# Kernel tuning notes

Measured on AMD Instinct MI355X. Metric: run time of the kernel, lower is better.

## Reference

```python
import jax, jax.numpy as jnp
import numpy as np

B, S_ENC, S_DEC, ENC_H, DEC_H = 8, 2048, 2048, 512, 512


def setup_inputs() -> dict:
    key = jax.random.key(0)
    k1, k2, k3 = jax.random.split(key, 3)
    return {
        "enc_hidden_states": jax.random.normal(k1, (B, S_ENC, ENC_H), dtype=jnp.float32),
        "dec_hidden_states": jax.random.normal(k2, (B, S_DEC, DEC_H), dtype=jnp.float32),
        "W_att": jax.random.normal(k3, (ENC_H, DEC_H), dtype=jnp.float32),
    }


def reference(enc_hidden_states, dec_hidden_states, W_att):
    # Project encoder states: [B, S_enc, dec_h]
    enc_proj = jnp.einsum("bse,ed->bsd", enc_hidden_states, W_att)
    # Luong 'general' scores for all decoder timesteps at once: [B, S_dec, S_enc]
    # (original code loops over decoder timesteps via tf.map_fn; this is the
    # equivalent single batched matmul)
    att_logits = jnp.einsum("btd,bsd->bts", dec_hidden_states, enc_proj)
    att_softmax = jax.nn.softmax(att_logits, axis=-1)
    # Attention context vectors: [B, S_dec, enc_h]
    att_vector = jnp.einsum("bts,bse->bte", att_softmax, enc_hidden_states)
    return att_vector
```

## Files before the change

kernel.cpp:

```cpp
#include <hip/hip_runtime.h>
#include <cstdint>


#define DEVINL __device__ __forceinline__

typedef __attribute__((ext_vector_type(8))) short short8;
typedef __attribute__((ext_vector_type(4))) float f32x4;

DEVINL short f2bf(float x) {
    union { float f; uint32_t u; } v; v.f = x;
    uint32_t r = v.u + 0x7FFFu + ((v.u >> 16) & 1u);
    return (short)(r >> 16);
}
DEVINL float bf2f(short h) {
    union { uint32_t u; float f; } v; v.u = ((uint32_t)(uint16_t)h) << 16;
    return v.f;
}

DEVINL void gload_lds16(const void* g, void* l) {
    __builtin_amdgcn_global_load_lds(
        (const __attribute__((address_space(1))) char*)g,
        (__attribute__((address_space(3))) char*)l, 16, 0, 0);
}

__global__ __launch_bounds__(256)
void split_kernel(const float* __restrict__ x, short* __restrict__ hi,
                  short* __restrict__ lo)
{
    long i = ((long)blockIdx.x * 256 + threadIdx.x) * 8;
    f32x4 a = *(const f32x4*)(x + i);
    f32x4 b = *(const f32x4*)(x + i + 4);
    short8 h, l;
#pragma unroll
    for (int j = 0; j < 4; j++) {
        short ha = f2bf(a[j]); h[j] = ha;     l[j] = f2bf(a[j] - bf2f(ha));
        short hb = f2bf(b[j]); h[4 + j] = hb; l[4 + j] = f2bf(b[j] - bf2f(hb));
    }
    *(short8*)(hi + i) = h;
    *(short8*)(lo + i) = l;
}

__global__ __launch_bounds__(256)
void split_w_kernel(const float* __restrict__ w, short* __restrict__ wth,
                    short* __restrict__ wtl)
{
    int idx = blockIdx.x * 256 + threadIdx.x;
    int k = idx >> 9, n = idx & 511;
    float v = w[idx];
    short h = f2bf(v);
    wth[(long)n * 512 + k] = h;
    wtl[(long)n * 512 + k] = f2bf(v - bf2f(h));
}

__global__ __launch_bounds__(256)
void split_transpose_kernel(const float* __restrict__ x, short* __restrict__ hi,
                            short* __restrict__ lo, short* __restrict__ xt)
{
    __shared__ short tile[32][33];
    const int b  = blockIdx.z;
    const int s0 = blockIdx.x * 32;
    const int e0 = blockIdx.y * 32;
    const float* px = x + (long)b * 2048 * 512;
    short* ph = hi + (long)b * 2048 * 512;
    short* pl = lo + (long)b * 2048 * 512;
    short* pt = xt + (long)b * 512 * 2048;
    const int tx = threadIdx.x & 31;
    const int ty = threadIdx.x >> 5;
#pragma unroll
    for (int r = 0; r < 32; r += 8) {
        long idx = (long)(s0 + ty + r) * 512 + e0 + tx;
        float v = px[idx];
        short h = f2bf(v);
        ph[idx] = h;
        pl[idx] = f2bf(v - bf2f(h));
        tile[ty + r][tx] = h;
    }
    __syncthreads();
#pragma unroll
    for (int r = 0; r < 32; r += 8)
        pt[(long)(e0 + ty + r) * 2048 + s0 + tx] = tile[tx][ty + r];
}

template<int NTERMS, bool SPLIT_OUT>
__global__ __launch_bounds__(256, 2)
void gemm_bt(const short* __restrict__ Ah, const short* __restrict__ Al,
             const short* __restrict__ Bh, const short* __restrict__ Bl,
             float* __restrict__ C, short* __restrict__ Ch, short* __restrict__ Cl,
             int K, int lda, int ldb, int ldc,
             long sA, long sB, long sC)
{
    extern __shared__ char smem_raw[];
    constexpr int OPS = (NTERMS == 3) ? 4 : 2;
    constexpr int SET = 128 * 32 * OPS;
    short* smem = (short*)smem_raw;

    const int tid  = threadIdx.x;
    const int wave = tid >> 6;
    const int lane = tid & 63;
    const int quad = lane >> 4;
    const int l16  = lane & 15;
    const int wm   = (wave >> 1) * 64;
    const int wn   = (wave & 1) * 64;

    const long tile_m = (long)blockIdx.y * 128;
    const long tile_n = (long)blockIdx.x * 128;
    const int  bz     = blockIdx.z;

    const short* pAh = Ah + (long)bz * sA;
    const short* pBh = Bh + (long)bz * sB;
    const short* pAl = (NTERMS == 3) ? (Al + (long)bz * sA) : nullptr;
    const short* pBl = (NTERMS == 3) ? (Bl + (long)bz * sB) : nullptr;

    const int srow = tid >> 2;
    const int skq  = (tid & 3) * 8;
    const int lds_off = srow * 32 + skq;
    const long ga0 = (tile_m + srow) * (long)lda + skq;
    const long gb0 = (tile_n + srow) * (long)ldb + skq;

    auto stage = [&](int k0, int buf) {
        short* s   = smem + buf * SET;
        short* ash = s;
        short* bsh = s + 128 * 32;
        gload_lds16(pAh + ga0 + k0,             ash + lds_off);
        gload_lds16(pAh + ga0 + 64l * lda + k0, ash + lds_off + 64 * 32);
        gload_lds16(pBh + gb0 + k0,             bsh + lds_off);
        gload_lds16(pBh + gb0 + 64l * ldb + k0, bsh + lds_off + 64 * 32);
        if constexpr (NTERMS == 3) {
            short* asl = s + 2 * 128 * 32;
            short* bsl = s + 3 * 128 * 32;
            gload_lds16(pAl + ga0 + k0,             asl + lds_off);
            gload_lds16(pAl + ga0 + 64l * lda + k0, asl + lds_off + 64 * 32);
            gload_lds16(pBl + gb0 + k0,             bsl + lds_off);
            gload_lds16(pBl + gb0 + 64l * ldb + k0, bsl + lds_off + 64 * 32);
        }
    };

    f32x4 acc[4][4] = {};
    stage(0, 0);
    int cur = 0;

    for (int k0 = 0; k0 < K; k0 += 32) {
        __syncthreads();
        if (k0 + 32 < K) stage(k0 + 32, cur ^ 1);

        short* s   = smem + cur * SET;
        short* ash = s;
        short* bsh = s + 128 * 32;
        short* asl = s + 2 * 128 * 32;
        short* bsl = s + 3 * 128 * 32;

        short8 ah[4], bh[4], al[4], bl[4];
#pragma unroll
        for (int i = 0; i < 4; i++) {
            ah[i] = *(const short8*)&ash[(wm + i * 16 + l16) * 32 + quad * 8];
            bh[i] = *(const short8*)&bsh[(wn + i * 16 + l16) * 32 + quad * 8];
            if constexpr (NTERMS == 3) {
                al[i] = *(const short8*)&asl[(wm + i * 16 + l16) * 32 + quad * 8];
                bl[i] = *(const short8*)&bsl[(wn + i * 16 + l16) * 32 + quad * 8];
            }
        }
#pragma unroll
        for (int i = 0; i < 4; i++)
#pragma unroll
            for (int j = 0; j < 4; j++) {
                acc[i][j] = __builtin_amdgcn_mfma_f32_16x16x32_bf16(ah[i], bh[j], acc[i][j], 0, 0, 0);
                if constexpr (NTERMS == 3) {
                    acc[i][j] = __builtin_amdgcn_mfma_f32_16x16x32_bf16(ah[i], bl[j], acc[i][j], 0, 0, 0);
                    acc[i][j] = __builtin_amdgcn_mfma_f32_16x16x32_bf16(al[i], bh[j], acc[i][j], 0, 0, 0);
                }
            }
        cur ^= 1;
    }

#pragma unroll
    for (int i = 0; i < 4; i++)
#pragma unroll
        for (int j = 0; j < 4; j++) {
            const long row0 = tile_m + wm + i * 16 + quad * 4;
            const long col  = tile_n + wn + j * 16 + l16;
#pragma unroll
            for (int r = 0; r < 4; r++) {
                float v = acc[i][j][r];
                if constexpr (SPLIT_OUT) {
                    long idx = (long)bz * sC + (row0 + r) * (long)ldc + col;
                    short h = f2bf(v);
                    Ch[idx] = h;
                    Cl[idx] = f2bf(v - bf2f(h));
                } else {
                    C[(long)bz * sC + (row0 + r) * (long)ldc + col] = v;
                }
            }
        }
}

__global__ __launch_bounds__(512, 2)
void gemm3_256(const short* __restrict__ Ah, const short* __restrict__ Al,
               const short* __restrict__ Bh, const short* __restrict__ Bl,
               float* __restrict__ C,
               int K, int lda, int ldb, int ldc,
               long sA, long sB, long sC, int nbx, int nby)
{
    extern __shared__ char smem_raw[];
    short* smem = (short*)smem_raw;
    constexpr int PL  = 256 * 32;
    constexpr int SET = 4 * PL;

    const int t    = threadIdx.x;
    const int wave = t >> 6;
    const int lane = t & 63;
    const int quad = lane >> 4;
    const int l16  = lane & 15;
    const int wm   = (wave >> 2) * 128;
    const int wn   = (wave & 3) * 64;
    const int kslot8 = ((quad ^ ((l16 >> 1) & 3)) << 3);

    const int nwg = gridDim.x;
    const int wg  = blockIdx.x;
    const int swz = (wg & 7) * (nwg >> 3) + (wg >> 3);
    const int per_b = nbx * nby;
    const int bz  = swz / per_b;
    const int rem = swz - bz * per_b;
    const long tile_m = (long)(rem / nbx) * 256;
    const long tile_n = (long)(rem % nbx) * 256;

    const short* pAh = Ah + (long)bz * sA;
    const short* pAl = Al + (long)bz * sA;
    const short* pBh = Bh + (long)bz * sB;
    const short* pBl = Bl + (long)bz * sB;

    const int srow   = t >> 2;
    const int schunk = (t & 3) ^ ((t >> 3) & 3);
    const long gA  = (tile_m + srow) * (long)lda + schunk * 8;
    const long gB  = (tile_n + srow) * (long)ldb + schunk * 8;
    const long gA2 = gA + 128l * lda;
    const long gB2 = gB + 128l * ldb;
    const int ld0 = t * 8;

    f32x4 acc[8][4] = {};

    {
        short* s = smem;
        gload_lds16(pAh + gA,  s + ld0);
        gload_lds16(pAh + gA2, s + ld0 + 4096);
        gload_lds16(pBh + gB,  s + 2 * PL + ld0);
        gload_lds16(pBh + gB2, s + 2 * PL + ld0 + 4096);
        gload_lds16(pAl + gA,  s + PL + ld0);
        gload_lds16(pAl + gA2, s + PL + ld0 + 4096);
        gload_lds16(pBl + gB,  s + 3 * PL + ld0);
        gload_lds16(pBl + gB2, s + 3 * PL + ld0 + 4096);
    }
    asm volatile("s_waitcnt vmcnt(4)" ::: "memory");
    __builtin_amdgcn_s_barrier();

    const int NT = K >> 5;
    int cur = 0;
#pragma unroll 1
    for (int kt = 0; kt < NT; ++kt) {
        const short* s    = smem + cur * SET;
        short* sn         = smem + (cur ^ 1) * SET;
        const short* ah_p = s;
        const short* al_p = s + PL;
        const short* bh_p = s + 2 * PL;
        const short* bl_p = s + 3 * PL;
        const int  k0n  = (kt + 1) << 5;
        const bool more = (kt + 1 < NT);

        short8 ahA[4], ahB[4], xbh[4], xbl[4], xal[4];

#pragma unroll
        for (int i = 0; i < 4; i++)
            ahA[i] = *(const short8*)&ah_p[(wm + i * 16 + l16) * 32 + kslot8];
#pragma unroll
        for (int j = 0; j < 4; j++)
            xbh[j] = *(const short8*)&bh_p[(wn + j * 16 + l16) * 32 + kslot8];
        if (more) {
            gload_lds16(pAh + gA  + k0n, sn + ld0);
            gload_lds16(pAh + gA2 + k0n, sn + ld0 + 4096);
        }
        __builtin_amdgcn_s_barrier();
        asm volatile("s_waitcnt lgkmcnt(0)" ::: "memory");
        __builtin_amdgcn_sched_barrier(0);
        __builtin_amdgcn_s_setprio(1);
#pragma unroll
        for (int i = 0; i < 4; i++)
#pragma unroll
            for (int j = 0; j < 4; j++)
                acc[i][j] = __builtin_amdgcn_mfma_f32_16x16x32_bf16(ahA[i], xbh[j], acc[i][j], 0, 0, 0);
        __builtin_amdgcn_s_setprio(0);

#pragma unroll
        for (int i = 0; i < 4; i++)
            ahB[i] = *(const short8*)&ah_p[(wm + 64 + i * 16 + l16) * 32 + kslot8];
        if (more) {
            gload_lds16(pBh + gB  + k0n, sn + 2 * PL + ld0);
            gload_lds16(pBh + gB2 + k0n, sn + 2 * PL + ld0 + 4096);
            asm volatile("s_waitcnt vmcnt(6)" ::: "memory");
        } else {
            asm volatile("s_waitcnt vmcnt(2)" ::: "memory");
        }
        __builtin_amdgcn_s_barrier();
        asm volatile("s_waitcnt lgkmcnt(0)" ::: "memory");
        __builtin_amdgcn_sched_barrier(0);
        __builtin_amdgcn_s_setprio(1);
#pragma unroll
        for (int i = 0; i < 4; i++)
#pragma unroll
            for (int j = 0; j < 4; j++)
                acc[4 + i][j] = __builtin_amdgcn_mfma_f32_16x16x32_bf16(ahB[i], xbh[j], acc[4 + i][j], 0, 0, 0);
        __builtin_amdgcn_s_setprio(0);

#pragma unroll
        for (int i = 0; i < 4; i++)
            xal[i] = *(const short8*)&al_p[(wm + i * 16 + l16) * 32 + kslot8];
        if (more) {
            gload_lds16(pAl + gA  + k0n, sn + PL + ld0);
            gload_lds16(pAl + gA2 + k0n, sn + PL + ld0 + 4096);
        }
        __builtin_amdgcn_s_barrier();
        asm volatile("s_waitcnt lgkmcnt(0)" ::: "memory");
        __builtin_amdgcn_sched_barrier(0);
        __builtin_amdgcn_s_setprio(1);
#pragma unroll
        for (int i = 0; i < 4; i++)
#pragma unroll
            for (int j = 0; j < 4; j++)
                acc[i][j] = __builtin_amdgcn_mfma_f32_16x16x32_bf16(xal[i], xbh[j], acc[i][j], 0, 0, 0);
        __builtin_amdgcn_s_setprio(0);

#pragma unroll
        for (int i = 0; i < 4; i++)
            xal[i] = *(const short8*)&al_p[(wm + 64 + i * 16 + l16) * 32 + kslot8];
        if (more) {
            gload_lds16(pBl + gB  + k0n, sn + 3 * PL + ld0);
            gload_lds16(pBl + gB2 + k0n, sn + 3 * PL + ld0 + 4096);
            asm volatile("s_waitcnt vmcnt(8)" ::: "memory");
        } else {
            asm volatile("s_waitcnt vmcnt(0)" ::: "memory");
        }
        __builtin_amdgcn_s_barrier();
        asm volatile("s_waitcnt lgkmcnt(0)" ::: "memory");
        __builtin_amdgcn_sched_barrier(0);
        __builtin_amdgcn_s_setprio(1);
#pragma unroll
        for (int i = 0; i < 4; i++)
#pragma unroll
            for (int j = 0; j < 4; j++)
                acc[4 + i][j] = __builtin_amdgcn_mfma_f32_16x16x32_bf16(xal[i], xbh[j], acc[4 + i][j], 0, 0, 0);
        __builtin_amdgcn_s_setprio(0);

#pragma unroll
        for (int j = 0; j < 4; j++)
            xbl[j] = *(const short8*)&bl_p[(wn + j * 16 + l16) * 32 + kslot8];
        __builtin_amdgcn_s_barrier();
        asm volatile("s_waitcnt lgkmcnt(0)" ::: "memory");
        __builtin_amdgcn_sched_barrier(0);
        __builtin_amdgcn_s_setprio(1);
#pragma unroll
        for (int i = 0; i < 4; i++)
#pragma unroll
            for (int j = 0; j < 4; j++)
                acc[i][j] = __builtin_amdgcn_mfma_f32_16x16x32_bf16(ahA[i], xbl[j], acc[i][j], 0, 0, 0);
        __builtin_amdgcn_s_setprio(0);

        __builtin_amdgcn_s_setprio(1);
#pragma unroll
        for (int i = 0; i < 4; i++)
#pragma unroll
            for (int j = 0; j < 4; j++)
                acc[4 + i][j] = __builtin_amdgcn_mfma_f32_16x16x32_bf16(ahB[i], xbl[j], acc[4 + i][j], 0, 0, 0);
        __builtin_amdgcn_s_setprio(0);
        if (more) {
            asm volatile("s_waitcnt vmcnt(4)" ::: "memory");
            __builtin_amdgcn_s_barrier();
        }

        cur ^= 1;
    }

#pragma unroll
    for (int i = 0; i < 8; i++)
#pragma unroll
        for (int j = 0; j < 4; j++) {
            const long row0 = tile_m + wm + i * 16 + quad * 4;
            const long col  = tile_n + wn + j * 16 + l16;
#pragma unroll
            for (int r = 0; r < 4; r++)
                C[(long)bz * sC + (row0 + r) * (long)ldc + col] = acc[i][j][r];
        }
}

__global__ __launch_bounds__(256)
void softmax_kernel(const float* __restrict__ logits, short* __restrict__ P)
{
    const long row = blockIdx.x;
    const float* p = logits + row * 2048;
    const int tid = threadIdx.x;
    const int lane = tid & 63, wave = tid >> 6;

    f32x4 v0 = *(const f32x4*)(p + tid * 8);
    f32x4 v1 = *(const f32x4*)(p + tid * 8 + 4);

    float m = fmaxf(fmaxf(fmaxf(v0[0], v0[1]), fmaxf(v0[2], v0[3])),
                    fmaxf(fmaxf(v1[0], v1[1]), fmaxf(v1[2], v1[3])));
#pragma unroll
    for (int o = 32; o > 0; o >>= 1) m = fmaxf(m, __shfl_xor(m, o));

    __shared__ float red[8];
    if (lane == 0) red[wave] = m;
    __syncthreads();
    m = fmaxf(fmaxf(red[0], red[1]), fmaxf(red[2], red[3]));

    float e[8];
    float s = 0.f;
#pragma unroll
    for (int i = 0; i < 4; i++) { e[i] = __expf(v0[i] - m); s += e[i]; }
#pragma unroll
    for (int i = 0; i < 4; i++) { e[4 + i] = __expf(v1[i] - m); s += e[4 + i]; }
#pragma unroll
    for (int o = 32; o > 0; o >>= 1) s += __shfl_xor(s, o);
    if (lane == 0) red[4 + wave] = s;
    __syncthreads();
    const float inv = 1.f / (red[4] + red[5] + red[6] + red[7]);

    short8 ob;
#pragma unroll
    for (int i = 0; i < 8; i++) ob[i] = f2bf(e[i] * inv);
    *(short8*)(P + row * 2048 + tid * 8) = ob;
}

extern "C" void kernel_launch(void* const* d_in, const int* in_sizes, int n_in,
                              void* d_out, int out_size, void* d_ws, size_t ws_size,
                              hipStream_t stream)
{
    const float* enc = (const float*)d_in[0];
    const float* dec = (const float*)d_in[1];
    const float* W   = (const float*)d_in[2];
    float* out = (float*)d_out;

    const long BSE = 8l * 2048 * 512;
    const long NW  = 512l * 512;

    char* p = (char*)d_ws;
    auto take = [&](long bytes) { char* r = p; p += (bytes + 255) & ~255l; return r; };
    short* enc_hi = (short*)take(BSE * 2);
    short* enc_lo = (short*)take(BSE * 2);
    short* dec_hi = (short*)take(BSE * 2);
    short* dec_lo = (short*)take(BSE * 2);
    short* ep_hi  = (short*)take(BSE * 2);
    short* ep_lo  = (short*)take(BSE * 2);
    short* enc_t  = (short*)take(BSE * 2);
    short* wt_hi  = (short*)take(NW * 2);
    short* wt_lo  = (short*)take(NW * 2);
    float* logits = (float*)take(8l * 2048 * 2048 * 4);
    short* Pbuf = enc_hi;
    (void)ws_size; (void)in_sizes; (void)n_in; (void)out_size;

    static bool attr_set = false;
    if (!attr_set) {
        (void)hipFuncSetAttribute((const void*)gemm3_256,
                                  hipFuncAttributeMaxDynamicSharedMemorySize,
                                  131072);
        attr_set = true;
    }

    split_transpose_kernel<<<dim3(64, 16, 8), 256, 0, stream>>>(
        enc, enc_hi, enc_lo, enc_t);
    split_kernel<<<4096, 256, 0, stream>>>(dec, dec_hi, dec_lo);
    split_w_kernel<<<1024, 256, 0, stream>>>(W, wt_hi, wt_lo);

    gemm_bt<3, true><<<dim3(4, 128, 1), 256, 64 * 1024, stream>>>(
        enc_hi, enc_lo, wt_hi, wt_lo, nullptr, ep_hi, ep_lo,
        512, 512, 512, 512, 0, 0, 0);

    gemm3_256<<<512, 512, 131072, stream>>>(
        dec_hi, dec_lo, ep_hi, ep_lo, logits,
        512, 512, 512, 2048, 2048l * 512, 2048l * 512, 2048l * 2048, 8, 8);

    softmax_kernel<<<16384, 256, 0, stream>>>(logits, Pbuf);

    gemm_bt<1, false><<<dim3(4, 16, 8), 256, 32 * 1024, stream>>>(
        Pbuf, nullptr, enc_t, nullptr, out, nullptr, nullptr,
        2048, 2048, 2048, 512, 2048l * 2048, 512l * 2048, 2048l * 512);
}
```

Baseline: 339.8 us.

## Fuse softmax into logits GEMM epilogue with per-tile stats and rescaled PV GEMM

The logits GEMM epilogue now computes a per-tile row max, writes unnormalized exp values as bf16 and stores per-tile (max, sum) stats, so the fp32 logits buffer and the separate softmax pass are no longer needed. A small combine kernel merges the eight per-tile stats for each row into scale factors. A new PV GEMM applies those scales to its partial accumulators every 256 columns of K. This removes a large fp32 write and read of the logits. In exchange the epilogue gains shuffles, barriers and scattered 2-byte stores, and it adds an extra kernel launch.

After: 319.5 us. -6.0%, faster.

```diff
diff --git a/kernel.cpp b/kernel.cpp
--- a/kernel.cpp
+++ b/kernel.cpp
@@ -196,9 +196,9 @@
 __global__ __launch_bounds__(512, 2)
 void gemm3_256(const short* __restrict__ Ah, const short* __restrict__ Al,
                const short* __restrict__ Bh, const short* __restrict__ Bl,
-               float* __restrict__ C,
-               int K, int lda, int ldb, int ldc,
-               long sA, long sB, long sC, int nbx, int nby)
+               short* __restrict__ Pt, float* __restrict__ stats,
+               int K, int lda, int ldb,
+               long sA, long sB, int nbx, int nby)
 {
     extern __shared__ char smem_raw[];
     short* smem = (short*)smem_raw;
@@ -377,55 +377,171 @@
         cur ^= 1;
     }
 
+    float* sf   = (float*)smem_raw;
+    float* lmax = sf;
+    float* rowm = sf + 1024;
+    const int wr = wave >> 2, wc = wave & 3;
+    __syncthreads();
+
 #pragma unroll
     for (int i = 0; i < 8; i++)
+#pragma unroll
+        for (int r = 0; r < 4; r++) {
+            float m = acc[i][0][r];
+#pragma unroll
+            for (int j = 1; j < 4; j++) m = fmaxf(m, acc[i][j][r]);
+#pragma unroll
+            for (int o = 1; o < 16; o <<= 1) m = fmaxf(m, __shfl_xor(m, o));
+            if (l16 == 0) lmax[wc * 256 + wr * 128 + i * 16 + quad * 4 + r] = m;
+        }
+    __syncthreads();
+    if (t < 256)
+        rowm[t] = fmaxf(fmaxf(lmax[t], lmax[256 + t]),
+                        fmaxf(lmax[512 + t], lmax[768 + t]));
+    __syncthreads();
+    float* lsum = sf;
+    short* PtB  = Pt + (long)bz * 2048 * 2048;
+#pragma unroll
+    for (int i = 0; i < 8; i++)
+#pragma unroll
+        for (int r = 0; r < 4; r++) {
+            const int rit = wr * 128 + i * 16 + quad * 4 + r;
+            const float m = rowm[rit];
+            float sum = 0.f;
+#pragma unroll
+            for (int j = 0; j < 4; j++) {
+                float e = __expf(acc[i][j][r] - m);
+                sum += e;
+                PtB[(tile_m + rit) * 2048 + tile_n + wn + j * 16 + l16] = f2bf(e);
+            }
+#pragma unroll
+            for (int o = 1; o < 16; o <<= 1) sum += __shfl_xor(sum, o);
+            if (l16 == 0) lsum[wc * 256 + rit] = sum;
+        }
+    __syncthreads();
+    if (t < 256) {
+        float S = lsum[t] + lsum[256 + t] + lsum[512 + t] + lsum[768 + t];
+        const long sidx = (((long)bz * 2048 + tile_m + t) * 8 + (tile_n >> 8)) * 2;
+        stats[sidx]     = rowm[t];
+        stats[sidx + 1] = S;
+    }
+}
+
+__global__ __launch_bounds__(256)
+void combine_kernel(const float* __restrict__ stats, float* __restrict__ scales)
+{
+    const long row = (long)blockIdx.x * 256 + threadIdx.x;
+    const float* p = stats + row * 16;
+    float m[8], s[8];
+#pragma unroll
+    for (int t = 0; t < 8; t++) { m[t] = p[t * 2]; s[t] = p[t * 2 + 1]; }
+    float M = m[0];
+#pragma unroll
+    for (int t = 1; t < 8; t++) M = fmaxf(M, m[t]);
+    float S = 0.f;
+#pragma unroll
+    for (int t = 0; t < 8; t++) S += s[t] * __expf(m[t] - M);
+    const float inv = 1.f / S;
+#pragma unroll
+    for (int t = 0; t < 8; t++)
+        scales[row * 8 + t] = __expf(m[t] - M) * inv;
+}
+
+__global__ __launch_bounds__(256, 2)
+void gemm_pv(const short* __restrict__ A, const short* __restrict__ B,
+             const float* __restrict__ scales, float* __restrict__ C,
+             int K, int lda, int ldb, int ldc,
+             long sA, long sB, long sC)
+{
+    extern __shared__ char smem_raw[];
+    constexpr int SET = 128 * 32 * 2;
+    short* smem = (short*)smem_raw;
+
+    const int tid  = threadIdx.x;
+    const int wave = tid >> 6;
+    const int lane = tid & 63;
+    const int quad = lane >> 4;
+    const int l16  = lane & 15;
+    const int wm   = (wave >> 1) * 64;
+    const int wn   = (wave & 1) * 64;
+
+    const long tile_m = (long)blockIdx.y * 128;
+    const long tile_n = (long)blockIdx.x * 128;
+    const int  bz     = blockIdx.z;
+
+    const short* pA = A + (long)bz * sA;
+    const short* pB = B + (long)bz * sB;
+
+    const int srow = tid >> 2;
+    const int skq  = (tid & 3) * 8;
+    const int lds_off = srow * 32 + skq;
+    const long ga0 = (tile_m + srow) * (long)lda + skq;
+    const long gb0 = (tile_n + srow) * (long)ldb + skq;
+
+    auto stage = [&](int k0, int buf) {
+        short* s   = smem + buf * SET;
+        short* ash = s;
+        short* bsh = s + 128 * 32;
+        gload_lds16(pA + ga0 + k0,             ash + lds_off);
+        gload_lds16(pA + ga0 + 64l * lda + k0, ash + lds_off + 64 * 32);
+        gload_lds16(pB + gb0 + k0,             bsh + lds_off);
+        gload_lds16(pB + gb0 + 64l * ldb + k0, bsh + lds_off + 64 * 32);
+    };
+
+    f32x4 acc[4][4] = {};
+    f32x4 oacc[4][4] = {};
+    const f32x4 vzero = {0.f, 0.f, 0.f, 0.f};
+    stage(0, 0);
+    int cur = 0;
+
+    for (int k0 = 0; k0 < K; k0 += 32) {
+        __syncthreads();
+        if (k0 + 32 < K) stage(k0 + 32, cur ^ 1);
+
+        short* s   = smem + cur * SET;
+        short* ash = s;
+        short* bsh = s + 128 * 32;
+
+        short8 ah[4], bh[4];
+#pragma unroll
+        for (int i = 0; i < 4; i++) {
+            ah[i] = *(const short8*)&ash[(wm + i * 16 + l16) * 32 + quad * 8];
+            bh[i] = *(const short8*)&bsh[(wn + i * 16 + l16) * 32 + quad * 8];
+        }
+#pragma unroll
+        for (int i = 0; i < 4; i++)
+#pragma unroll
+            for (int j = 0; j < 4; j++)
+                acc[i][j] = __builtin_amdgcn_mfma_f32_16x16x32_bf16(ah[i], bh[j], acc[i][j], 0, 0, 0);
+
+        if (((k0 + 32) & 255) == 0) {
+            const int tt = k0 >> 8;
+#pragma unroll
+            for (int i = 0; i < 4; i++) {
+                f32x4 sv;
+#pragma unroll
+                for (int r = 0; r < 4; r++)
+                    sv[r] = scales[((long)bz * 2048 + tile_m + wm + i * 16 + quad * 4 + r) * 8 + tt];
+#pragma unroll
+                for (int j = 0; j < 4; j++) {
+                    oacc[i][j] += sv * acc[i][j];
+                    acc[i][j] = vzero;
+                }
+            }
+        }
+        cur ^= 1;
+    }
+
+#pragma unroll
+    for (int i = 0; i < 4; i++)
 #pragma unroll
         for (int j = 0; j < 4; j++) {
             const long row0 = tile_m + wm + i * 16 + quad * 4;
             const long col  = tile_n + wn + j * 16 + l16;
 #pragma unroll
             for (int r = 0; r < 4; r++)
-                C[(long)bz * sC + (row0 + r) * (long)ldc + col] = acc[i][j][r];
-        }
-}
-
-__global__ __launch_bounds__(256)
-void softmax_kernel(const float* __restrict__ logits, short* __restrict__ P)
-{
-    const long row = blockIdx.x;
-    const float* p = logits + row * 2048;
-    const int tid = threadIdx.x;
-    const int lane = tid & 63, wave = tid >> 6;
-
-    f32x4 v0 = *(const f32x4*)(p + tid * 8);
-    f32x4 v1 = *(const f32x4*)(p + tid * 8 + 4);
-
-    float m = fmaxf(fmaxf(fmaxf(v0[0], v0[1]), fmaxf(v0[2], v0[3])),
-                    fmaxf(fmaxf(v1[0], v1[1]), fmaxf(v1[2], v1[3])));
-#pragma unroll
-    for (int o = 32; o > 0; o >>= 1) m = fmaxf(m, __shfl_xor(m, o));
-
-    __shared__ float red[8];
-    if (lane == 0) red[wave] = m;
-    __syncthreads();
-    m = fmaxf(fmaxf(red[0], red[1]), fmaxf(red[2], red[3]));
-
-    float e[8];
-    float s = 0.f;
-#pragma unroll
-    for (int i = 0; i < 4; i++) { e[i] = __expf(v0[i] - m); s += e[i]; }
-#pragma unroll
-    for (int i = 0; i < 4; i++) { e[4 + i] = __expf(v1[i] - m); s += e[4 + i]; }
-#pragma unroll
-    for (int o = 32; o > 0; o >>= 1) s += __shfl_xor(s, o);
-    if (lane == 0) red[4 + wave] = s;
-    __syncthreads();
-    const float inv = 1.f / (red[4] + red[5] + red[6] + red[7]);
-
-    short8 ob;
-#pragma unroll
-    for (int i = 0; i < 8; i++) ob[i] = f2bf(e[i] * inv);
-    *(short8*)(P + row * 2048 + tid * 8) = ob;
+                C[(long)bz * sC + (row0 + r) * (long)ldc + col] = oacc[i][j][r];
+        }
 }
 
 extern "C" void kernel_launch(void* const* d_in, const int* in_sizes, int n_in,
@@ -451,8 +567,9 @@
     short* enc_t  = (short*)take(BSE * 2);
     short* wt_hi  = (short*)take(NW * 2);
     short* wt_lo  = (short*)take(NW * 2);
-    float* logits = (float*)take(8l * 2048 * 2048 * 4);
-    short* Pbuf = enc_hi;
+    short* Pt     = (short*)take(8l * 2048 * 2048 * 2);
+    float* stats  = (float*)take(8l * 2048 * 8 * 2 * 4);
+    float* scales = (float*)take(8l * 2048 * 8 * 4);
     (void)ws_size; (void)in_sizes; (void)n_in; (void)out_size;
 
     static bool attr_set = false;
@@ -473,12 +590,12 @@
         512, 512, 512, 512, 0, 0, 0);
 
     gemm3_256<<<512, 512, 131072, stream>>>(
-        dec_hi, dec_lo, ep_hi, ep_lo, logits,
-        512, 512, 512, 2048, 2048l * 512, 2048l * 512, 2048l * 2048, 8, 8);
-
-    softmax_kernel<<<16384, 256, 0, stream>>>(logits, Pbuf);
-
-    gemm_bt<1, false><<<dim3(4, 16, 8), 256, 32 * 1024, stream>>>(
-        Pbuf, nullptr, enc_t, nullptr, out, nullptr, nullptr,
+        dec_hi, dec_lo, ep_hi, ep_lo, Pt, stats,
+        512, 512, 512, 2048l * 512, 2048l * 512, 8, 8);
+
+    combine_kernel<<<64, 256, 0, stream>>>(stats, scales);
+
+    gemm_pv<<<dim3(4, 16, 8), 256, 32 * 1024, stream>>>(
+        Pt, enc_t, scales, out,
         2048, 2048, 2048, 512, 2048l * 2048, 512l * 2048, 2048l * 512);
 }
```
